# Optimization experiments

Measured on AMD Instinct MI355X. Metric: run time of the kernel, lower is better.

Reference implementation:

```python
import jax, jax.numpy as jnp
import numpy as np

NUM_IMGS = 16
MASKS_PER_IMG = 8   # masks per image (one annotation group per image)
REGION_TOKENS = 4   # region_token_num


def setup_inputs() -> dict:
    key = jax.random.key(0)
    k1, k2, k3, k4, k5, k6 = jax.random.split(key, 6)
    C_in, C_hid = 1024, 4096
    feats = jax.random.normal(k1, (NUM_IMGS * MASKS_PER_IMG, 576, C_in), jnp.float32)
    masks = jax.random.normal(k2, (NUM_IMGS, MASKS_PER_IMG, 336, 336), jnp.float32)
    W1 = jax.random.normal(k3, (C_in, C_hid), jnp.float32) * (1.0 / np.sqrt(C_in))
    b1 = jax.random.normal(k4, (C_hid,), jnp.float32) * 0.02
    W2 = jax.random.normal(k5, (C_hid, C_hid), jnp.float32) * (1.0 / np.sqrt(C_hid))
    b2 = jax.random.normal(k6, (C_hid,), jnp.float32) * 0.02
    return {"feats": feats, "masks": masks, "W1": W1, "b1": b1, "W2": W2, "b2": b2}


def _token_merge(x, r, num_out):
    # x: [n, d]; merge contiguous runs of high-similarity tokens down to num_out tokens
    nrm = x / jnp.maximum(jnp.linalg.norm(x, axis=-1, keepdims=True), 1e-12)
    sim = jnp.sum(nrm[:-1] * nrm[1:], axis=-1)          # [n-1]
    vals, _ = jax.lax.top_k(sim, r)
    kth = vals[-1]                                      # r-th largest similarity
    cut = (sim < kth).astype(jnp.int32)                 # boundary after token i
    seg = jnp.concatenate([jnp.zeros((1,), jnp.int32), jnp.cumsum(cut)])  # [n]
    sums = jax.ops.segment_sum(x, seg, num_segments=num_out)
    counts = jax.ops.segment_sum(jnp.ones((x.shape[0],), x.dtype), seg, num_segments=num_out)
    return sums / jnp.maximum(counts, 1.0)[:, None]     # [num_out, d]


def reference(feats, masks, W1, b1, W2, b2):
    num_imgs, M, H, W = masks.shape
    P, C = feats.shape[1], feats.shape[2]
    N = int(round(P ** 0.5))                            # 24
    feats_g = feats.reshape(num_imgs, M, N, N, C)       # grouped per image

    def per_image(feat, mask):
        # feat: [M, N, N, C], mask: [M, H, W]
        m = jax.image.resize(mask, (M, N, N), method="bilinear")  # align_corners=False semantics
        m = (m > 0).astype(feat.dtype)
        denorm = m.sum(axis=(-1, -2)) + 1e-8            # [M]
        pooled = jnp.einsum("mijc,mij->mc", feat, m) / denorm[:, None]  # [M, C]
        return _token_merge(pooled, M - REGION_TOKENS, REGION_TOKENS)    # [R, C]

    merged = jax.vmap(per_image)(feats_g, masks)        # [num_imgs, R, C]
    tokens = merged.reshape(-1, C)                      # [num_imgs*R, C]
    h = jax.nn.gelu(tokens @ W1 + b1, approximate=False)
    return h @ W2 + b2
```

## Files before the change

### kernel.cpp

```cpp
#include <hip/hip_runtime.h>
#include <hip/hip_bf16.h>
#include <math.h>

#define NIMG 16
#define MPI  8
#define NPAIR 128
#define RTOK 4
#define HW_  336
#define NN_  24
#define P_   576
#define C_   1024
#define CH_  4096
#define NTOK 64
#define TAPS 28
#define TAPS_P 29
#define PSLICE 8
#define S1 8
#define S2 16

__device__ __forceinline__ int wstart(int o){ int s = 14*o - 7; return s < 0 ? 0 : s; }

__global__ __launch_bounds__(256) void k_mask(const float* __restrict__ masks,
                                              unsigned short* __restrict__ actIdx,
                                              int* __restrict__ cnt) {
  int pair = blockIdx.x;
  const float* gm = masks + (size_t)pair * (HW_*HW_);
  __shared__ float wW[NN_][TAPS_P];
  __shared__ float T[HW_][NN_];
  __shared__ int lcnt;
  int tid = threadIdx.x;

  if (tid < NN_) {
    int o = tid;
    int st = wstart(o);
    float s_o = 14.0f*(float)o + 6.5f;
    float tmp[TAPS];
    float sum = 0.f;
    for (int t = 0; t < TAPS; t++) {
      int p = st + t;
      float w = 0.f;
      if (p < HW_) {
        float x = fabsf((float)p - s_o) * (1.0f/14.0f);
        w = fmaxf(0.f, 1.f - x);
      }
      tmp[t] = w; sum += w;
    }
    float inv = 1.0f / sum;
    for (int t = 0; t < TAPS; t++) wW[o][t] = tmp[t]*inv;
  }
  if (tid == 0) lcnt = 0;
  __syncthreads();

  for (int idx = tid; idx < HW_*NN_; idx += 256) {
    int r = idx / NN_, oc = idx % NN_;
    int st = wstart(oc);
    const float* row = gm + r*HW_;
    float s = 0.f;
    #pragma unroll
    for (int t = 0; t < TAPS; t++) {
      int p = st + t;
      if (p < HW_) s += wW[oc][t] * row[p];
    }
    T[r][oc] = s;
  }
  __syncthreads();

  for (int idx = tid; idx < NN_*NN_; idx += 256) {
    int oh = idx / NN_, ow = idx % NN_;
    int st = wstart(oh);
    float s = 0.f;
    #pragma unroll
    for (int t = 0; t < TAPS; t++) {
      int r = st + t;
      if (r < HW_) s += wW[oh][t] * T[r][ow];
    }
    if (s > 0.f) {
      int pos = atomicAdd(&lcnt, 1);
      actIdx[(size_t)pair*P_ + pos] = (unsigned short)idx;
    }
  }
  __syncthreads();
  if (tid == 0) cnt[pair] = lcnt;
}

__global__ __launch_bounds__(256) void k_pool(const float* __restrict__ feats,
                                              const unsigned short* __restrict__ actIdx,
                                              const int* __restrict__ cnt,
                                              float* __restrict__ poolPart) {
  int slice = blockIdx.x & (PSLICE-1);
  int pair  = blockIdx.x / PSLICE;
  int n  = cnt[pair];
  int lo = (n * slice) / PSLICE;
  int hi = (n * (slice+1)) / PSLICE;
  int tid = threadIdx.x;
  const unsigned short* ai = actIdx + (size_t)pair*P_;
  const float* fb = feats + (size_t)pair * P_ * C_ + 4*tid;
  float4 acc = make_float4(0.f, 0.f, 0.f, 0.f);
  for (int i = lo; i < hi; i++) {
    const float4 v = *(const float4*)(fb + (size_t)ai[i]*C_);
    acc.x += v.x; acc.y += v.y; acc.z += v.z; acc.w += v.w;
  }
  *(float4*)(poolPart + ((size_t)slice*NPAIR + pair)*C_ + 4*tid) = acc;
}

__global__ __launch_bounds__(256) void k_merge(const float* __restrict__ poolPart,
                                               const int* __restrict__ cnt,
                                               float* __restrict__ tokT) {
  int img = blockIdx.x;
  int tid = threadIdx.x;
  int wv = tid >> 6, ln = tid & 63;
  __shared__ float pool[MPI][C_];
  __shared__ float nrm[MPI][C_];
  __shared__ float norms[MPI];
  __shared__ float sims[MPI];
  __shared__ int seg[MPI];

  for (int idx = tid; idx < MPI*C_; idx += 256) {
    int m_ = idx >> 10, c = idx & (C_-1);
    int pair = img*MPI + m_;
    float s = 0.f;
    #pragma unroll
    for (int sl = 0; sl < PSLICE; sl++)
      s += poolPart[((size_t)sl*NPAIR + pair)*C_ + c];
    pool[m_][c] = s / ((float)cnt[pair] + 1e-8f);
  }
  __syncthreads();

  for (int h = 0; h < 2; h++) {
    int m_ = wv*2 + h;
    float s = 0.f;
    for (int c = ln; c < C_; c += 64) { float v = pool[m_][c]; s += v*v; }
    for (int o = 32; o > 0; o >>= 1) s += __shfl_xor(s, o);
    if (ln == 0) norms[m_] = fmaxf(sqrtf(s), 1e-12f);
  }
  __syncthreads();

  for (int idx = tid; idx < MPI*C_; idx += 256) {
    int m_ = idx >> 10, c = idx & (C_-1);
    nrm[m_][c] = pool[m_][c] / norms[m_];
  }
  __syncthreads();

  for (int h = 0; h < 2; h++) {
    int i = wv + h*4;
    if (i < MPI-1) {
      float s = 0.f;
      for (int c = ln; c < C_; c += 64) s += nrm[i][c]*nrm[i+1][c];
      for (int o = 32; o > 0; o >>= 1) s += __shfl_xor(s, o);
      if (ln == 0) sims[i] = s;
    }
  }
  __syncthreads();

  if (tid == 0) {
    float v[MPI-1];
    for (int i = 0; i < MPI-1; i++) v[i] = sims[i];
    for (int i = 1; i < MPI-1; i++) {
      float key = v[i]; int j = i-1;
      while (j >= 0 && v[j] < key) { v[j+1] = v[j]; j--; }
      v[j+1] = key;
    }
    float kth = v[RTOK-1];
    int s = 0; seg[0] = 0;
    for (int i = 1; i < MPI; i++) { if (sims[i-1] < kth) s++; seg[i] = s; }
  }
  __syncthreads();

  for (int idx = tid; idx < RTOK*C_; idx += 256) {
    int r = idx >> 10, c = idx & (C_-1);
    float s = 0.f; int k = 0;
    #pragma unroll
    for (int m_ = 0; m_ < MPI; m_++) {
      if (seg[m_] == r) { s += pool[m_][c]; k++; }
    }
    tokT[(size_t)c*NTOK + img*RTOK + r] = s / fmaxf((float)k, 1.0f);
  }
}

#define FMA4(ACC,AV) ACC.x=fmaf(AV,w.x,ACC.x);ACC.y=fmaf(AV,w.y,ACC.y);ACC.z=fmaf(AV,w.z,ACC.z);ACC.w=fmaf(AV,w.w,ACC.w)
__global__ __launch_bounds__(64) void k_gemm(const float* __restrict__ AT,
                                             const float* __restrict__ W,
                                             float* __restrict__ part,
                                             int N, int KS) {
  int ln = threadIdx.x;
  int mi = ln >> 4;
  int ji = ln & 15;
  int jc = blockIdx.x*64 + ji*4;
  int k0 = blockIdx.y*KS;
  float4 acc[16];
  #pragma unroll
  for (int r = 0; r < 16; r++) acc[r] = make_float4(0.f,0.f,0.f,0.f);

  const float* ap = AT + (size_t)k0*NTOK + mi*16;
  const float* wp = W  + (size_t)k0*N + jc;
  for (int k = 0; k < KS; k++) {
    float4 w  = *(const float4*)(wp);
    float4 a0 = *(const float4*)(ap);
    float4 a1 = *(const float4*)(ap+4);
    float4 a2 = *(const float4*)(ap+8);
    float4 a3 = *(const float4*)(ap+12);
    wp += N; ap += NTOK;
    FMA4(acc[0], a0.x); FMA4(acc[1], a0.y); FMA4(acc[2], a0.z); FMA4(acc[3], a0.w);
    FMA4(acc[4], a1.x); FMA4(acc[5], a1.y); FMA4(acc[6], a1.z); FMA4(acc[7], a1.w);
    FMA4(acc[8], a2.x); FMA4(acc[9], a2.y); FMA4(acc[10],a2.z); FMA4(acc[11],a2.w);
    FMA4(acc[12],a3.x); FMA4(acc[13],a3.y); FMA4(acc[14],a3.z); FMA4(acc[15],a3.w);
  }
  #pragma unroll
  for (int q = 0; q < 4; q++)
    #pragma unroll
    for (int r = 0; r < 4; r++) {
      int row = mi*16 + q*4 + r;
      *(float4*)(part + ((size_t)blockIdx.y*NTOK + row)*N + jc) = acc[q*4+r];
    }
}

__global__ __launch_bounds__(256) void k_reduce1(const float* __restrict__ part,
                                                 const float* __restrict__ b1,
                                                 float* __restrict__ hT) {
  __shared__ float tile[64][65];
  int j0 = blockIdx.x * 64;
  int tid = threadIdx.x;
  for (int i = tid; i < 64*64; i += 256) {
    int m = i >> 6, jj = i & 63;
    float s = 0.f;
    #pragma unroll
    for (int ss = 0; ss < S1; ss++) s += part[((size_t)ss*NTOK + m)*CH_ + j0 + jj];
    s += b1[j0 + jj];
    float g = 0.5f * s * (1.0f + erff(s * 0.70710678118654752f));
    tile[jj][m] = g;
  }
  __syncthreads();
  for (int i = tid; i < 64*64; i += 256) {
    int jj = i >> 6, m = i & 63;
    hT[(size_t)(j0 + jj)*NTOK + m] = tile[jj][m];
  }
}

__global__ __launch_bounds__(256) void k_reduce2(const float* __restrict__ part,
                                                 const float* __restrict__ b2,
                                                 float* __restrict__ out) {
  int idx = blockIdx.x*256 + threadIdx.x;
  float s = 0.f;
  #pragma unroll
  for (int ss = 0; ss < S2; ss++) s += part[(size_t)ss*NTOK*CH_ + idx];
  out[idx] = s + b2[idx & (CH_-1)];
}

extern "C" void kernel_launch(void* const* d_in, const int* in_sizes, int n_in,
                              void* d_out, int out_size, void* d_ws, size_t ws_size,
                              hipStream_t stream) {
  (void)in_sizes; (void)n_in; (void)out_size; (void)ws_size;
  const float* feats = (const float*)d_in[0];
  const float* masks = (const float*)d_in[1];
  const float* W1    = (const float*)d_in[2];
  const float* b1    = (const float*)d_in[3];
  const float* W2    = (const float*)d_in[4];
  const float* b2    = (const float*)d_in[5];
  float* out = (float*)d_out;
  char* ws = (char*)d_ws;

  unsigned short* actIdx = (unsigned short*)(ws + 0);
  int*   cnt      = (int*)  (ws + 147456);
  float* poolPart = (float*)(ws + 147968);
  float* tokT     = (float*)(ws + 4342272);
  float* g1part   = (float*)(ws + 4604416);
  float* hT       = (float*)(ws + 12993024);
  float* g2part   = (float*)(ws + 14041600);

  k_mask <<<NPAIR, 256, 0, stream>>>(masks, actIdx, cnt);
  k_pool <<<NPAIR*PSLICE, 256, 0, stream>>>(feats, actIdx, cnt, poolPart);
  k_merge<<<NIMG, 256, 0, stream>>>(poolPart, cnt, tokT);
  k_gemm <<<dim3(CH_/64, S1), 64, 0, stream>>>(tokT, W1, g1part, CH_, C_/S1);
  k_reduce1<<<CH_/64, 256, 0, stream>>>(g1part, b1, hT);
  k_gemm <<<dim3(CH_/64, S2), 64, 0, stream>>>(hT, W2, g2part, CH_, CH_/S2);
  k_reduce2<<<(NTOK*CH_)/256, 256, 0, stream>>>(g2part, b2, out);
}
```

Measured before the change: 740.5 us.

## Split mask resize into grid-wide kernel, unroll pooling, prefetch GEMM weights

Splits the mask resize, which used one block per mask pair, into a horizontal pass spread across 1024 blocks (writing to a global buffer) and a vertical pass that loads that buffer into shared memory. The pooling gather is unrolled by 8 to keep more loads in flight, and the merge reduction now uses float4 loads. The GEMM register-double-buffers eight rows of weights ahead, and the first GEMM's K split goes from 8 to 16 for more blocks. The cost is an extra launch plus a round trip through global memory for the intermediate, a larger partial-sum buffer, and higher register pressure in the GEMM.

```diff
diff --git a/kernel.cpp b/kernel.cpp
--- a/kernel.cpp
+++ b/kernel.cpp
@@ -13,66 +13,71 @@
 #define CH_  4096
 #define NTOK 64
 #define TAPS 28
-#define TAPS_P 29
 #define PSLICE 8
-#define S1 8
+#define S1 16
 #define S2 16
 
 __device__ __forceinline__ int wstart(int o){ int s = 14*o - 7; return s < 0 ? 0 : s; }
 
-__global__ __launch_bounds__(256) void k_mask(const float* __restrict__ masks,
-                                              unsigned short* __restrict__ actIdx,
-                                              int* __restrict__ cnt) {
-  int pair = blockIdx.x;
-  const float* gm = masks + (size_t)pair * (HW_*HW_);
-  __shared__ float wW[NN_][TAPS_P];
-  __shared__ float T[HW_][NN_];
-  __shared__ int lcnt;
-  int tid = threadIdx.x;
-
-  if (tid < NN_) {
-    int o = tid;
-    int st = wstart(o);
-    float s_o = 14.0f*(float)o + 6.5f;
-    float tmp[TAPS];
-    float sum = 0.f;
+__global__ __launch_bounds__(256) void k_resizeW(const float* __restrict__ masks,
+                                                 float* __restrict__ Tg) {
+  int gsz = gridDim.x * 256;
+  for (int idx = blockIdx.x*256 + threadIdx.x; idx < NPAIR*HW_*NN_; idx += gsz) {
+    int oc = idx % NN_;
+    int rowIdx = idx / NN_;
+    const float* row = masks + (size_t)rowIdx * HW_;
+    int st = wstart(oc);
+    float s_o = 14.0f*(float)oc + 6.5f;
+    float wt[TAPS];
+    float wsum = 0.f;
+    #pragma unroll
     for (int t = 0; t < TAPS; t++) {
       int p = st + t;
-      float w = 0.f;
-      if (p < HW_) {
-        float x = fabsf((float)p - s_o) * (1.0f/14.0f);
-        w = fmaxf(0.f, 1.f - x);
-      }
-      tmp[t] = w; sum += w;
-    }
-    float inv = 1.0f / sum;
-    for (int t = 0; t < TAPS; t++) wW[o][t] = tmp[t]*inv;
-  }
+      float w = (p < HW_) ? fmaxf(0.f, 1.f - fabsf((float)p - s_o)*(1.0f/14.0f)) : 0.f;
+      wt[t] = w; wsum += w;
+    }
+    float inv = 1.0f / wsum;
+    float s = 0.f;
+    #pragma unroll
+    for (int t = 0; t < TAPS; t++) {
+      int p = st + t; p = (p < HW_) ? p : (HW_-1);
+      s += (wt[t]*inv) * row[p];
+    }
+    Tg[idx] = s;
+  }
+}
+
+__global__ __launch_bounds__(256) void k_resizeH(const float* __restrict__ Tg,
+                                                 unsigned short* __restrict__ actIdx,
+                                                 int* __restrict__ cnt) {
+  int pair = blockIdx.x;
+  int tid = threadIdx.x;
+  __shared__ float T[HW_*NN_];
+  __shared__ int lcnt;
+  const float4* src = (const float4*)(Tg + (size_t)pair*HW_*NN_);
+  float4* dst = (float4*)T;
+  for (int i = tid; i < HW_*NN_/4; i += 256) dst[i] = src[i];
   if (tid == 0) lcnt = 0;
   __syncthreads();
 
-  for (int idx = tid; idx < HW_*NN_; idx += 256) {
-    int r = idx / NN_, oc = idx % NN_;
-    int st = wstart(oc);
-    const float* row = gm + r*HW_;
-    float s = 0.f;
-    #pragma unroll
-    for (int t = 0; t < TAPS; t++) {
-      int p = st + t;
-      if (p < HW_) s += wW[oc][t] * row[p];
-    }
-    T[r][oc] = s;
-  }
-  __syncthreads();
-
-  for (int idx = tid; idx < NN_*NN_; idx += 256) {
+  for (int idx = tid; idx < P_; idx += 256) {
     int oh = idx / NN_, ow = idx % NN_;
     int st = wstart(oh);
-    float s = 0.f;
+    float s_o = 14.0f*(float)oh + 6.5f;
+    float wt[TAPS];
+    float wsum = 0.f;
     #pragma unroll
     for (int t = 0; t < TAPS; t++) {
       int r = st + t;
-      if (r < HW_) s += wW[oh][t] * T[r][ow];
+      float w = (r < HW_) ? fmaxf(0.f, 1.f - fabsf((float)r - s_o)*(1.0f/14.0f)) : 0.f;
+      wt[t] = w; wsum += w;
+    }
+    float inv = 1.0f / wsum;
+    float s = 0.f;
+    #pragma unroll
+    for (int t = 0; t < TAPS; t++) {
+      int r = st + t; r = (r < HW_) ? r : (HW_-1);
+      s += (wt[t]*inv) * T[r*NN_ + ow];
     }
     if (s > 0.f) {
       int pos = atomicAdd(&lcnt, 1);
@@ -96,7 +101,28 @@
   const unsigned short* ai = actIdx + (size_t)pair*P_;
   const float* fb = feats + (size_t)pair * P_ * C_ + 4*tid;
   float4 acc = make_float4(0.f, 0.f, 0.f, 0.f);
-  for (int i = lo; i < hi; i++) {
+  int i = lo;
+  for (; i + 8 <= hi; i += 8) {
+    int r0 = ai[i+0], r1 = ai[i+1], r2 = ai[i+2], r3 = ai[i+3];
+    int r4 = ai[i+4], r5 = ai[i+5], r6 = ai[i+6], r7 = ai[i+7];
+    float4 v0 = *(const float4*)(fb + (size_t)r0*C_);
+    float4 v1 = *(const float4*)(fb + (size_t)r1*C_);
+    float4 v2 = *(const float4*)(fb + (size_t)r2*C_);
+    float4 v3 = *(const float4*)(fb + (size_t)r3*C_);
+    float4 v4 = *(const float4*)(fb + (size_t)r4*C_);
+    float4 v5 = *(const float4*)(fb + (size_t)r5*C_);
+    float4 v6 = *(const float4*)(fb + (size_t)r6*C_);
+    float4 v7 = *(const float4*)(fb + (size_t)r7*C_);
+    acc.x += v0.x; acc.y += v0.y; acc.z += v0.z; acc.w += v0.w;
+    acc.x += v1.x; acc.y += v1.y; acc.z += v1.z; acc.w += v1.w;
+    acc.x += v2.x; acc.y += v2.y; acc.z += v2.z; acc.w += v2.w;
+    acc.x += v3.x; acc.y += v3.y; acc.z += v3.z; acc.w += v3.w;
+    acc.x += v4.x; acc.y += v4.y; acc.z += v4.z; acc.w += v4.w;
+    acc.x += v5.x; acc.y += v5.y; acc.z += v5.z; acc.w += v5.w;
+    acc.x += v6.x; acc.y += v6.y; acc.z += v6.z; acc.w += v6.w;
+    acc.x += v7.x; acc.y += v7.y; acc.z += v7.z; acc.w += v7.w;
+  }
+  for (; i < hi; i++) {
     const float4 v = *(const float4*)(fb + (size_t)ai[i]*C_);
     acc.x += v.x; acc.y += v.y; acc.z += v.z; acc.w += v.w;
   }
@@ -115,14 +141,18 @@
   __shared__ float sims[MPI];
   __shared__ int seg[MPI];
 
-  for (int idx = tid; idx < MPI*C_; idx += 256) {
-    int m_ = idx >> 10, c = idx & (C_-1);
+  for (int idx = tid; idx < MPI*C_/4; idx += 256) {
+    int m_ = idx >> 8, q = idx & 255;
     int pair = img*MPI + m_;
-    float s = 0.f;
-    #pragma unroll
-    for (int sl = 0; sl < PSLICE; sl++)
-      s += poolPart[((size_t)sl*NPAIR + pair)*C_ + c];
-    pool[m_][c] = s / ((float)cnt[pair] + 1e-8f);
+    float4 s = make_float4(0.f,0.f,0.f,0.f);
+    #pragma unroll
+    for (int sl = 0; sl < PSLICE; sl++) {
+      float4 v = *(const float4*)(poolPart + ((size_t)sl*NPAIR + pair)*C_ + q*4);
+      s.x += v.x; s.y += v.y; s.z += v.z; s.w += v.w;
+    }
+    float inv = 1.0f / ((float)cnt[pair] + 1e-8f);
+    pool[m_][q*4+0] = s.x * inv; pool[m_][q*4+1] = s.y * inv;
+    pool[m_][q*4+2] = s.z * inv; pool[m_][q*4+3] = s.w * inv;
   }
   __syncthreads();
 
@@ -191,19 +221,32 @@
   #pragma unroll
   for (int r = 0; r < 16; r++) acc[r] = make_float4(0.f,0.f,0.f,0.f);
 
-  const float* ap = AT + (size_t)k0*NTOK + mi*16;
-  const float* wp = W  + (size_t)k0*N + jc;
-  for (int k = 0; k < KS; k++) {
-    float4 w  = *(const float4*)(wp);
-    float4 a0 = *(const float4*)(ap);
-    float4 a1 = *(const float4*)(ap+4);
-    float4 a2 = *(const float4*)(ap+8);
-    float4 a3 = *(const float4*)(ap+12);
-    wp += N; ap += NTOK;
-    FMA4(acc[0], a0.x); FMA4(acc[1], a0.y); FMA4(acc[2], a0.z); FMA4(acc[3], a0.w);
-    FMA4(acc[4], a1.x); FMA4(acc[5], a1.y); FMA4(acc[6], a1.z); FMA4(acc[7], a1.w);
-    FMA4(acc[8], a2.x); FMA4(acc[9], a2.y); FMA4(acc[10],a2.z); FMA4(acc[11],a2.w);
-    FMA4(acc[12],a3.x); FMA4(acc[13],a3.y); FMA4(acc[14],a3.z); FMA4(acc[15],a3.w);
+  const float* ap    = AT + (size_t)k0*NTOK + mi*16;
+  const float* wbase = W  + (size_t)k0*N + jc;
+  const float* wp    = wbase;
+  float4 wbuf[8];
+  #pragma unroll
+  for (int kk = 0; kk < 8; kk++) wbuf[kk] = *(const float4*)(wp + (size_t)kk*N);
+  wp += 8*(size_t)N;
+
+  for (int k8 = 0; k8 < KS; k8 += 8) {
+    bool more = (k8 + 8) < KS;
+    const float* pre = more ? wp : wbase;
+    #pragma unroll
+    for (int kk = 0; kk < 8; kk++) {
+      float4 a0 = *(const float4*)(ap);
+      float4 a1 = *(const float4*)(ap+4);
+      float4 a2 = *(const float4*)(ap+8);
+      float4 a3 = *(const float4*)(ap+12);
+      ap += NTOK;
+      float4 w = wbuf[kk];
+      FMA4(acc[0], a0.x); FMA4(acc[1], a0.y); FMA4(acc[2], a0.z); FMA4(acc[3], a0.w);
+      FMA4(acc[4], a1.x); FMA4(acc[5], a1.y); FMA4(acc[6], a1.z); FMA4(acc[7], a1.w);
+      FMA4(acc[8], a2.x); FMA4(acc[9], a2.y); FMA4(acc[10],a2.z); FMA4(acc[11],a2.w);
+      FMA4(acc[12],a3.x); FMA4(acc[13],a3.y); FMA4(acc[14],a3.z); FMA4(acc[15],a3.w);
+      wbuf[kk] = *(const float4*)(pre + (size_t)kk*N);
+    }
+    wp += 8*(size_t)N;
   }
   #pragma unroll
   for (int q = 0; q < 4; q++)
@@ -261,13 +304,15 @@
 
   unsigned short* actIdx = (unsigned short*)(ws + 0);
   int*   cnt      = (int*)  (ws + 147456);
-  float* poolPart = (float*)(ws + 147968);
-  float* tokT     = (float*)(ws + 4342272);
-  float* g1part   = (float*)(ws + 4604416);
-  float* hT       = (float*)(ws + 12993024);
-  float* g2part   = (float*)(ws + 14041600);
-
-  k_mask <<<NPAIR, 256, 0, stream>>>(masks, actIdx, cnt);
+  float* Tg       = (float*)(ws + 147968);
+  float* poolPart = (float*)(ws + 4276736);
+  float* tokT     = (float*)(ws + 8471040);
+  float* g1part   = (float*)(ws + 8733184);
+  float* hT       = (float*)(ws + 25510400);
+  float* g2part   = (float*)(ws + 26558976);
+
+  k_resizeW<<<1024, 256, 0, stream>>>(masks, Tg);
+  k_resizeH<<<NPAIR, 256, 0, stream>>>(Tg, actIdx, cnt);
   k_pool <<<NPAIR*PSLICE, 256, 0, stream>>>(feats, actIdx, cnt, poolPart);
   k_merge<<<NIMG, 256, 0, stream>>>(poolPart, cnt, tokT);
   k_gemm <<<dim3(CH_/64, S1), 64, 0, stream>>>(tokT, W1, g1part, CH_, C_/S1);
```

New measurement: 666.3 us. 10.0% less time.
